# Kernel tuning notes

Hardware: AMD Instinct MI355X
Metric: run time of the kernel (lower is better)

The kernel has to match this reference:

```python
import jax, jax.numpy as jnp
import numpy as np


def _split_feature(x, ns):
    # channel-last split: [b,h,w,c] -> [b*ns*ns, h/ns, w/ns, c]
    b, h, w, c = x.shape
    hn, wn = h // ns, w // ns
    return x.reshape(b, ns, hn, ns, wn, c).transpose(0, 1, 3, 2, 4, 5).reshape(b * ns * ns, hn, wn, c)


def _merge_splits(x, ns):
    # inverse of _split_feature: [b*ns*ns, h, w, c] -> [b, ns*h, ns*w, c]
    b, h, w, c = x.shape
    nb = b // (ns * ns)
    return x.reshape(nb, ns, ns, h, w, c).transpose(0, 1, 3, 2, 4, 5).reshape(nb, ns * h, ns * w, c)


def _gen_shift_window_attn_mask(h, w, ns):
    # numpy replica of _unimatch_generate_shift_window_attn_mask
    wsh, wsw = h // ns, w // ns
    ssh, ssw = wsh // 2, wsw // 2
    img = np.zeros((1, h, w, 1), dtype=np.float32)
    cnt = 0
    for hs in (slice(0, -wsh), slice(-wsh, -ssh), slice(-ssh, None)):
        for ws in (slice(0, -wsw), slice(-wsw, -ssw), slice(-ssw, None)):
            img[:, hs, ws, :] = cnt
            cnt += 1
    win = img.reshape(1, ns, wsh, ns, wsw, 1).transpose(0, 1, 3, 2, 4, 5).reshape(ns * ns, wsh * wsw)
    am = win[:, None, :] - win[:, :, None]
    return np.where(am != 0, np.float32(-100.0), np.float32(0.0)).astype(np.float32)


def setup_inputs() -> dict:
    key = jax.random.key(0)
    B, H, W, C, NS = 8, 96, 128, 128, 4
    kq, kk, kv = jax.random.split(key, 3)
    q = jax.random.normal(kq, (B, H * W, C), jnp.float32)
    k = jax.random.normal(kk, (B, H * W, C), jnp.float32)
    v = jax.random.normal(kv, (B, H * W, C), jnp.float32)
    attn_mask = jnp.asarray(_gen_shift_window_attn_mask(H, W, NS))  # [NS*NS, n, n]
    return {"q": q, "k": k, "v": v, "attn_mask": attn_mask,
            "num_splits": NS, "with_shift": 1, "h": H, "w": W}


def reference(q, k, v, attn_mask, num_splits, with_shift, h, w):
    b, _, c = q.shape
    ns = num_splits
    wsh, wsw = h // ns, w // ns
    n = wsh * wsw
    bn = b * ns * ns
    q = q.reshape(b, h, w, c)
    k = k.reshape(b, h, w, c)
    v = v.reshape(b, h, w, c)
    if with_shift:
        sh, sw = wsh // 2, wsw // 2
        q = jnp.roll(q, (-sh, -sw), axis=(1, 2))
        k = jnp.roll(k, (-sh, -sw), axis=(1, 2))
        v = jnp.roll(v, (-sh, -sw), axis=(1, 2))
    qf = _split_feature(q, ns).reshape(bn, n, c)
    kf = _split_feature(k, ns).reshape(bn, n, c)
    vf = _split_feature(v, ns).reshape(bn, n, c)
    scale = jnp.asarray(c, qf.dtype) ** 0.5
    scores = jnp.einsum('bnc,bmc->bnm', qf, kf) / scale  # [bn, n, n]
    if with_shift:
        scores = scores + jnp.tile(attn_mask, (b, 1, 1))
    attn = jax.nn.softmax(scores, axis=-1)
    out = jnp.einsum('bnm,bmc->bnc', attn, vf)
    out = _merge_splits(out.reshape(bn, wsh, wsw, c), ns)  # [b, h, w, c]
    if with_shift:
        out = jnp.roll(out, (sh, sw), axis=(1, 2))
    return out.reshape(b, h * w, c)
```

## Files before the change

### kernel.cpp

```cpp
#include <hip/hip_runtime.h>

#define H 96
#define W 128
#define C 128
#define WSH 24
#define WSW 32
#define NTOK 768
#define SH 12
#define SW 16
#define KT 32
#define NKT 24
#define PSTR 40
#define TILE_USH 8192
#define WS_NEED (128L * NKT * TILE_USH * 2)

typedef __attribute__((ext_vector_type(8))) short short8;
typedef __attribute__((ext_vector_type(4))) float floatx4;

__device__ inline unsigned short f2bf(float f) {
  union { float f; unsigned u; } un; un.f = f;
  unsigned r = un.u + 0x7FFF + ((un.u >> 16) & 1);
  return (unsigned short)(r >> 16);
}

__device__ inline int tok_off(int tok, int wh, int ww) {
  int r = tok >> 5;
  int cc = tok & 31;
  int y = wh * WSH + r + SH; if (y >= H) y -= H;
  int x = ww * WSW + cc + SW; if (x >= W) x -= W;
  return y * W + x;
}

__global__ __launch_bounds__(256) void prep_kernel(const float* __restrict__ k,
                                                   const float* __restrict__ v,
                                                   unsigned short* __restrict__ ws) {
  __shared__ unsigned short Vlds[KT][136];
  const int bid = blockIdx.x;
  const int w = bid / NKT;
  const int kt = bid - w * NKT;
  const int batch = w >> 4, win = w & 15;
  const int wh = win >> 2, ww = win & 3;
  int y = wh * WSH + kt + SH; if (y >= H) y -= H;

  const int t = threadIdx.x;
  const int key = t >> 3;
  const int j = t & 7;
  const int c0 = j * 16;
  int x = ww * WSW + key + SW; if (x >= W) x -= W;
  const long src = ((long)batch * H * W + (long)y * W + x) * C + c0;
  unsigned short* tile = ws + (long)bid * TILE_USH;

  {
    const float* kp = k + src;
    short8 s0, s1;
#pragma unroll
    for (int i = 0; i < 2; ++i) {
      floatx4 a = *(const floatx4*)(kp + i * 8);
      floatx4 b = *(const floatx4*)(kp + i * 8 + 4);
      s0[i*4+0] = (short)f2bf(a[0]); s0[i*4+1] = (short)f2bf(a[1]);
      s0[i*4+2] = (short)f2bf(a[2]); s0[i*4+3] = (short)f2bf(a[3]);
      s1[i*4+0] = (short)f2bf(b[0]); s1[i*4+1] = (short)f2bf(b[1]);
      s1[i*4+2] = (short)f2bf(b[2]); s1[i*4+3] = (short)f2bf(b[3]);
    }
    short8 o0, o1;
    o0[0]=s0[0]; o0[1]=s0[1]; o0[2]=s0[2]; o0[3]=s0[3]; o0[4]=s1[0]; o0[5]=s1[1]; o0[6]=s1[2]; o0[7]=s1[3];
    o1[0]=s0[4]; o1[1]=s0[5]; o1[2]=s0[6]; o1[3]=s0[7]; o1[4]=s1[4]; o1[5]=s1[5]; o1[6]=s1[6]; o1[7]=s1[7];
    const int kc = j >> 1;
    const int q2 = (j & 1) * 2;
    unsigned short* kout = tile + kc * 1024 + key * 32 + q2 * 8;
    *(short8*)(kout) = o0;
    *(short8*)(kout + 8) = o1;
  }
  {
    const float* vp = v + src;
#pragma unroll
    for (int i = 0; i < 4; ++i) {
      floatx4 a = *(const floatx4*)(vp + i * 4);
      Vlds[key][c0 + i*4 + 0] = f2bf(a[0]);
      Vlds[key][c0 + i*4 + 1] = f2bf(a[1]);
      Vlds[key][c0 + i*4 + 2] = f2bf(a[2]);
      Vlds[key][c0 + i*4 + 3] = f2bf(a[3]);
    }
  }
  __syncthreads();
  {
    const int cb = t >> 5;
    const int rem = t & 31;
    const int col = rem >> 1, qh = rem & 1;
    const int ch = cb * 16 + col;
#pragma unroll
    for (int qs = 0; qs < 2; ++qs) {
      const int quad = qh * 2 + qs;
      short8 o;
#pragma unroll
      for (int i = 0; i < 8; ++i)
        o[i] = (short)Vlds[(i & 1) * 16 + quad * 4 + (i >> 1)][ch];
      *(short8*)(tile + 4096 + cb * 512 + (col * 4 + quad) * 8) = o;
    }
  }
}

__global__ __launch_bounds__(128, 2) void attn_main(const float* __restrict__ q,
                                                    const unsigned short* __restrict__ ws,
                                                    float* __restrict__ out) {
  __shared__ unsigned short Ps[2][3][16 * PSTR];

  const int bid = blockIdx.x;
  const int x8 = bid & 7;
  const int i = bid >> 3;
  const int w = x8 * 16 + (i & 15);
  const int qb = i >> 4;
  const int batch = w >> 4, win = w & 15;
  const int wh = win >> 2, ww = win & 3;

  const int tid = threadIdx.x;
  const int wave = tid >> 6, lane = tid & 63;
  const int col = lane & 15, quad = lane >> 4;
  const long bbase = (long)batch * (H * W * C);
  const int qbase = qb * 96 + wave * 48;
  const int loff = (col * 4 + quad) * 8;

  short8 qfrag[3][4];
#pragma unroll
  for (int s = 0; s < 3; ++s) {
    const int qtok = qbase + s * 16 + col;
    const float* qp = q + bbase + (long)tok_off(qtok, wh, ww) * C + quad * 8;
#pragma unroll
    for (int kc = 0; kc < 4; ++kc) {
      floatx4 a = *(const floatx4*)(qp + kc * 32);
      floatx4 b = *(const floatx4*)(qp + kc * 32 + 4);
      short8 v8;
      v8[0]=(short)f2bf(a[0]); v8[1]=(short)f2bf(a[1]); v8[2]=(short)f2bf(a[2]); v8[3]=(short)f2bf(a[3]);
      v8[4]=(short)f2bf(b[0]); v8[5]=(short)f2bf(b[1]); v8[6]=(short)f2bf(b[2]); v8[7]=(short)f2bf(b[3]);
      qfrag[s][kc] = v8;
    }
  }

  int qreg[3];
#pragma unroll
  for (int s = 0; s < 3; ++s) {
    int t0 = qbase + s * 16;
    int rr_s = t0 >> 5;
    int qh = (wh == 3) ? ((rr_s >= SH) ? 2 : 1) : 0;
    int qw = (ww == 3) ? ((t0 & 16) ? 2 : 1) : 0;
    qreg[s] = qh * 3 + qw;
  }
  const int cw0 = (ww == 3) ? 1 : 0, cw1 = (ww == 3) ? 2 : 0;
  const float MNEG = -144.2695041f;
  const float SC2 = 0.12751739f;

  floatx4 oacc[3][8];
#pragma unroll
  for (int s = 0; s < 3; ++s)
#pragma unroll
    for (int cb = 0; cb < 8; ++cb) oacc[s][cb] = (floatx4){0.f, 0.f, 0.f, 0.f};
  float lsum[3][4];
#pragma unroll
  for (int s = 0; s < 3; ++s)
#pragma unroll
    for (int r = 0; r < 4; ++r) lsum[s][r] = 0.f;

  const unsigned short* wsw_ = ws + (long)w * (NKT * TILE_USH);

  short8 kf0[4], kf1[4];
  auto load_k = [&](int kt) {
    const unsigned short* tk = wsw_ + ((long)kt << 13);
#pragma unroll
    for (int kc = 0; kc < 4; ++kc) {
      kf0[kc] = *(const short8*)(tk + kc * 1024 + loff);
      kf1[kc] = *(const short8*)(tk + kc * 1024 + 512 + loff);
    }
  };
  load_k(0);

  for (int kt = 0; kt < NKT; ++kt) {
    const unsigned short* tv = wsw_ + ((long)kt << 13) + 4096;
    short8 vf[8];
#pragma unroll
    for (int cb = 0; cb < 8; ++cb) vf[cb] = *(const short8*)(tv + cb * 512 + loff);

    const int khb = (wh == 3) ? ((kt >= SH) ? 6 : 3) : 0;
    const int kr0 = khb + cw0, kr1 = khb + cw1;

#pragma unroll
    for (int s = 0; s < 3; ++s) {
      floatx4 a0 = (floatx4){0.f, 0.f, 0.f, 0.f};
      floatx4 a1 = (floatx4){0.f, 0.f, 0.f, 0.f};
#pragma unroll
      for (int kc = 0; kc < 4; ++kc) {
        a0 = __builtin_amdgcn_mfma_f32_16x16x32_bf16(qfrag[s][kc], kf0[kc], a0, 0, 0, 0);
        a1 = __builtin_amdgcn_mfma_f32_16x16x32_bf16(qfrag[s][kc], kf1[kc], a1, 0, 0, 0);
      }
      const float m0 = (qreg[s] == kr0) ? 0.f : MNEG;
      const float m1 = (qreg[s] == kr1) ? 0.f : MNEG;
#pragma unroll
      for (int r = 0; r < 4; ++r) {
        float p0 = __builtin_amdgcn_exp2f(fmaf(a0[r], SC2, m0));
        float p1 = __builtin_amdgcn_exp2f(fmaf(a1[r], SC2, m1));
        lsum[s][r] += p0 + p1;
        unsigned pk = (unsigned)f2bf(p0) | ((unsigned)f2bf(p1) << 16);
        *(unsigned*)&Ps[wave][s][(quad * 4 + r) * PSTR + 2 * col] = pk;
      }
    }

    if (kt + 1 < NKT) load_k(kt + 1);

#pragma unroll
    for (int s = 0; s < 3; ++s) {
      short8 pf = *(const short8*)&Ps[wave][s][col * PSTR + quad * 8];
#pragma unroll
      for (int cb = 0; cb < 8; ++cb)
        oacc[s][cb] = __builtin_amdgcn_mfma_f32_16x16x32_bf16(pf, vf[cb], oacc[s][cb], 0, 0, 0);
    }
  }

#pragma unroll
  for (int s = 0; s < 3; ++s)
#pragma unroll
    for (int r = 0; r < 4; ++r) {
      float l = lsum[s][r];
      l += __shfl_xor(l, 1); l += __shfl_xor(l, 2);
      l += __shfl_xor(l, 4); l += __shfl_xor(l, 8);
      float inv = 1.0f / l;
      int tok = qbase + s * 16 + quad * 4 + r;
      float* op = out + bbase + (long)tok_off(tok, wh, ww) * C + col;
#pragma unroll
      for (int cb = 0; cb < 8; ++cb) op[cb * 16] = oacc[s][cb][r] * inv;
    }
}

#define KSTRF 136
#define VSTRF 40
#define PSTRF 40
__global__ __launch_bounds__(256, 2) void attn_fallback(
    const float* __restrict__ q, const float* __restrict__ k,
    const float* __restrict__ v, const float* __restrict__ mask,
    float* __restrict__ out) {
  __shared__ unsigned short Ks[KT * KSTRF];
  __shared__ unsigned short Vtl[C * VSTRF];
  __shared__ unsigned short Psf[4][16 * PSTRF];
  const int qtile = blockIdx.x;
  const int beta  = blockIdx.y;
  const int batch = beta >> 4;
  const int win   = beta & 15;
  const int wh = win >> 2, ww = win & 3;
  const int tid = threadIdx.x;
  const int wave = tid >> 6, lane = tid & 63;
  const int col = lane & 15, quad = lane >> 4;
  const long bbase = (long)batch * (H * W * C);
  const int qtok = qtile * 64 + wave * 16 + col;
  const float* qp = q + bbase + (long)tok_off(qtok, wh, ww) * C + quad * 8;
  short8 qfrag[4];
#pragma unroll
  for (int kc = 0; kc < 4; ++kc) {
    floatx4 a = *(const floatx4*)(qp + kc * 32);
    floatx4 b = *(const floatx4*)(qp + kc * 32 + 4);
    short8 s;
    s[0]=f2bf(a[0]); s[1]=f2bf(a[1]); s[2]=f2bf(a[2]); s[3]=f2bf(a[3]);
    s[4]=f2bf(b[0]); s[5]=f2bf(b[1]); s[6]=f2bf(b[2]); s[7]=f2bf(b[3]);
    qfrag[kc] = s;
  }
  floatx4 oacc[8];
#pragma unroll
  for (int i = 0; i < 8; ++i) oacc[i] = (floatx4){0.f,0.f,0.f,0.f};
  float mrow[4], lrow[4];
#pragma unroll
  for (int r = 0; r < 4; ++r) { mrow[r] = -1e30f; lrow[r] = 0.f; }
  const int skey = tid >> 3;
  const int sch  = (tid & 7) * 4;
  const float invscale = 0.088388347648318447f;
  const float* maskw = mask + (long)win * (NTOK * NTOK);
  const int qrow_m = qtile * 64 + wave * 16 + quad * 4;
  for (int kt = 0; kt < NKT; ++kt) {
    const int ktok0 = kt * KT;
    const long srow = bbase + (long)tok_off(ktok0 + skey, wh, ww) * C;
    const float* kp = k + srow;
    const float* vp = v + srow;
    __syncthreads();
#pragma unroll
    for (int j = 0; j < 4; ++j) {
      floatx4 f = *(const floatx4*)(kp + sch + j * 32);
      unsigned lo = (unsigned)f2bf(f[0]) | ((unsigned)f2bf(f[1]) << 16);
      unsigned hi = (unsigned)f2bf(f[2]) | ((unsigned)f2bf(f[3]) << 16);
      *(uint2*)&Ks[skey * KSTRF + sch + j * 32] = make_uint2(lo, hi);
    }
#pragma unroll
    for (int j = 0; j < 4; ++j) {
      floatx4 f = *(const floatx4*)(vp + sch + j * 32);
      int chb = sch + j * 32;
      Vtl[(chb + 0) * VSTRF + skey] = f2bf(f[0]);
      Vtl[(chb + 1) * VSTRF + skey] = f2bf(f[1]);
      Vtl[(chb + 2) * VSTRF + skey] = f2bf(f[2]);
      Vtl[(chb + 3) * VSTRF + skey] = f2bf(f[3]);
    }
    __syncthreads();
    floatx4 s0 = (floatx4){0.f,0.f,0.f,0.f};
    floatx4 s1 = (floatx4){0.f,0.f,0.f,0.f};
#pragma unroll
    for (int kc = 0; kc < 4; ++kc) {
      short8 k0 = *(const short8*)&Ks[col * KSTRF + kc * 32 + quad * 8];
      short8 k1 = *(const short8*)&Ks[(col + 16) * KSTRF + kc * 32 + quad * 8];
      s0 = __builtin_amdgcn_mfma_f32_16x16x32_bf16(qfrag[kc], k0, s0, 0, 0, 0);
      s1 = __builtin_amdgcn_mfma_f32_16x16x32_bf16(qfrag[kc], k1, s1, 0, 0, 0);
    }
    float mk0[4], mk1[4];
    const float* mp = maskw + (long)qrow_m * NTOK + ktok0 + col;
#pragma unroll
    for (int r = 0; r < 4; ++r) { mk0[r] = mp[r * NTOK]; mk1[r] = mp[r * NTOK + 16]; }
#pragma unroll
    for (int r = 0; r < 4; ++r) {
      float a0 = s0[r] * invscale + mk0[r];
      float a1 = s1[r] * invscale + mk1[r];
      float mx = fmaxf(a0, a1);
      mx = fmaxf(mx, __shfl_xor(mx, 1)); mx = fmaxf(mx, __shfl_xor(mx, 2));
      mx = fmaxf(mx, __shfl_xor(mx, 4)); mx = fmaxf(mx, __shfl_xor(mx, 8));
      float mnew = fmaxf(mrow[r], mx);
      float alpha = __expf(mrow[r] - mnew);
      float p0 = __expf(a0 - mnew);
      float p1 = __expf(a1 - mnew);
      float rs = p0 + p1;
      rs += __shfl_xor(rs, 1); rs += __shfl_xor(rs, 2);
      rs += __shfl_xor(rs, 4); rs += __shfl_xor(rs, 8);
      lrow[r] = lrow[r] * alpha + rs;
      mrow[r] = mnew;
#pragma unroll
      for (int cb = 0; cb < 8; ++cb) oacc[cb][r] *= alpha;
      Psf[wave][(quad * 4 + r) * PSTRF + col]      = f2bf(p0);
      Psf[wave][(quad * 4 + r) * PSTRF + 16 + col] = f2bf(p1);
    }
    __syncthreads();
    short8 pf = *(const short8*)&Psf[wave][col * PSTRF + quad * 8];
#pragma unroll
    for (int cb = 0; cb < 8; ++cb) {
      short8 vf = *(const short8*)&Vtl[(cb * 16 + col) * VSTRF + quad * 8];
      oacc[cb] = __builtin_amdgcn_mfma_f32_16x16x32_bf16(pf, vf, oacc[cb], 0, 0, 0);
    }
  }
#pragma unroll
  for (int r = 0; r < 4; ++r) {
    float inv_l = 1.0f / lrow[r];
    int tok = qtile * 64 + wave * 16 + quad * 4 + r;
    float* op = out + bbase + (long)tok_off(tok, wh, ww) * C + col;
#pragma unroll
    for (int cb = 0; cb < 8; ++cb) op[cb * 16] = oacc[cb][r] * inv_l;
  }
}

extern "C" void kernel_launch(void* const* d_in, const int* in_sizes, int n_in,
                              void* d_out, int out_size, void* d_ws, size_t ws_size,
                              hipStream_t stream) {
  const float* q    = (const float*)d_in[0];
  const float* k    = (const float*)d_in[1];
  const float* v    = (const float*)d_in[2];
  const float* mask = (const float*)d_in[3];
  float* out = (float*)d_out;
  if (ws_size >= (size_t)WS_NEED) {
    prep_kernel<<<128 * NKT, 256, 0, stream>>>(k, v, (unsigned short*)d_ws);
    attn_main<<<1024, 128, 0, stream>>>(q, (const unsigned short*)d_ws, out);
  } else {
    attn_fallback<<<dim3(12, 128), dim3(256), 0, stream>>>(q, k, v, mask, out);
  }
}
```

Before: 252.9 us.

## Stage K/V tiles into LDS via async global_load_lds with double buffering

The attention kernel now uses 4-wave blocks covering 192 queries. Each key tile (K and V bf16, 16KB) is loaded once per block into double-buffered LDS with global_load_lds, replacing per-wave global loads, and a barrier is placed at the end of each iteration. The prep kernel's block-to-window mapping is remapped so that each XCD handles the same windows, which should improve L2 locality. In exchange the kernel uses more LDS per block, halves the grid to 512 blocks, and waits on vmcnt(0) plus a barrier every iteration, which may serialize the prefetch.

```diff
diff --git a/kernel.cpp b/kernel.cpp
--- a/kernel.cpp
+++ b/kernel.cpp
@@ -31,13 +31,21 @@
   return y * W + x;
 }
 
+__device__ inline void gll16(const void* g, void* lds) {
+  __builtin_amdgcn_global_load_lds(
+      (const __attribute__((address_space(1))) unsigned int*)g,
+      (__attribute__((address_space(3))) unsigned int*)lds, 16, 0, 0);
+}
+
 __global__ __launch_bounds__(256) void prep_kernel(const float* __restrict__ k,
                                                    const float* __restrict__ v,
                                                    unsigned short* __restrict__ ws) {
   __shared__ unsigned short Vlds[KT][136];
   const int bid = blockIdx.x;
-  const int w = bid / NKT;
-  const int kt = bid - w * NKT;
+  const int xcd = bid & 7;
+  const int jj = bid >> 3;
+  const int w = xcd * 16 + (jj & 15);
+  const int kt = jj >> 4;
   const int batch = w >> 4, win = w & 15;
   const int wh = win >> 2, ww = win & 3;
   int y = wh * WSH + kt + SH; if (y >= H) y -= H;
@@ -48,7 +56,7 @@
   const int c0 = j * 16;
   int x = ww * WSW + key + SW; if (x >= W) x -= W;
   const long src = ((long)batch * H * W + (long)y * W + x) * C + c0;
-  unsigned short* tile = ws + (long)bid * TILE_USH;
+  unsigned short* tile = ws + ((long)w * NKT + kt) * TILE_USH;
 
   {
     const float* kp = k + src;
@@ -100,10 +108,11 @@
   }
 }
 
-__global__ __launch_bounds__(128, 2) void attn_main(const float* __restrict__ q,
+__global__ __launch_bounds__(256, 2) void attn_main(const float* __restrict__ q,
                                                     const unsigned short* __restrict__ ws,
                                                     float* __restrict__ out) {
-  __shared__ unsigned short Ps[2][3][16 * PSTR];
+  __shared__ unsigned short Kv[2][TILE_USH];
+  __shared__ unsigned short Ps[4][3][16 * PSTR];
 
   const int bid = blockIdx.x;
   const int x8 = bid & 7;
@@ -114,11 +123,24 @@
   const int wh = win >> 2, ww = win & 3;
 
   const int tid = threadIdx.x;
-  const int wave = tid >> 6, lane = tid & 63;
+  const int wv = tid >> 6, lane = tid & 63;
   const int col = lane & 15, quad = lane >> 4;
   const long bbase = (long)batch * (H * W * C);
-  const int qbase = qb * 96 + wave * 48;
+  const int qbase = qb * 192 + wv * 48;
   const int loff = (col * 4 + quad) * 8;
+
+  const char* wtile = (const char*)(ws + (long)w * (NKT * TILE_USH));
+
+  auto stage = [&](int buf, int kt) {
+    const char* g = wtile + ((long)kt << 14);
+#pragma unroll
+    for (int c = 0; c < 4; ++c) {
+      const int chunk = wv * 4 + c;
+      gll16(g + chunk * 1024 + lane * 16, &Kv[buf][chunk * 512]);
+    }
+  };
+
+  stage(0, 0);
 
   short8 qfrag[3][4];
 #pragma unroll
@@ -160,24 +182,19 @@
 #pragma unroll
     for (int r = 0; r < 4; ++r) lsum[s][r] = 0.f;
 
-  const unsigned short* wsw_ = ws + (long)w * (NKT * TILE_USH);
-
-  short8 kf0[4], kf1[4];
-  auto load_k = [&](int kt) {
-    const unsigned short* tk = wsw_ + ((long)kt << 13);
+  asm volatile("s_waitcnt vmcnt(0)" ::: "memory");
+  __builtin_amdgcn_s_barrier();
+
+  for (int kt = 0; kt < NKT; ++kt) {
+    const int cur = kt & 1;
+    if (kt + 1 < NKT) stage(cur ^ 1, kt + 1);
+
+    short8 kf0[4], kf1[4];
 #pragma unroll
     for (int kc = 0; kc < 4; ++kc) {
-      kf0[kc] = *(const short8*)(tk + kc * 1024 + loff);
-      kf1[kc] = *(const short8*)(tk + kc * 1024 + 512 + loff);
-    }
-  };
-  load_k(0);
-
-  for (int kt = 0; kt < NKT; ++kt) {
-    const unsigned short* tv = wsw_ + ((long)kt << 13) + 4096;
-    short8 vf[8];
-#pragma unroll
-    for (int cb = 0; cb < 8; ++cb) vf[cb] = *(const short8*)(tv + cb * 512 + loff);
+      kf0[kc] = *(const short8*)&Kv[cur][kc * 1024 + loff];
+      kf1[kc] = *(const short8*)&Kv[cur][kc * 1024 + 512 + loff];
+    }
 
     const int khb = (wh == 3) ? ((kt >= SH) ? 6 : 3) : 0;
     const int kr0 = khb + cw0, kr1 = khb + cw1;
@@ -199,18 +216,26 @@
         float p1 = __builtin_amdgcn_exp2f(fmaf(a1[r], SC2, m1));
         lsum[s][r] += p0 + p1;
         unsigned pk = (unsigned)f2bf(p0) | ((unsigned)f2bf(p1) << 16);
-        *(unsigned*)&Ps[wave][s][(quad * 4 + r) * PSTR + 2 * col] = pk;
+        *(unsigned*)&Ps[wv][s][(quad * 4 + r) * PSTR + 2 * col] = pk;
       }
     }
 
-    if (kt + 1 < NKT) load_k(kt + 1);
+    short8 vf[8];
+#pragma unroll
+    for (int cb = 0; cb < 8; ++cb)
+      vf[cb] = *(const short8*)&Kv[cur][4096 + cb * 512 + loff];
 
 #pragma unroll
     for (int s = 0; s < 3; ++s) {
-      short8 pf = *(const short8*)&Ps[wave][s][col * PSTR + quad * 8];
+      short8 pf = *(const short8*)&Ps[wv][s][col * PSTR + quad * 8];
 #pragma unroll
       for (int cb = 0; cb < 8; ++cb)
         oacc[s][cb] = __builtin_amdgcn_mfma_f32_16x16x32_bf16(pf, vf[cb], oacc[s][cb], 0, 0, 0);
+    }
+
+    if (kt + 1 < NKT) {
+      asm volatile("s_waitcnt vmcnt(0)" ::: "memory");
+      __builtin_amdgcn_s_barrier();
     }
   }
 
@@ -356,7 +381,7 @@
   float* out = (float*)d_out;
   if (ws_size >= (size_t)WS_NEED) {
     prep_kernel<<<128 * NKT, 256, 0, stream>>>(k, v, (unsigned short*)d_ws);
-    attn_main<<<1024, 128, 0, stream>>>(q, (const unsigned short*)d_ws, out);
+    attn_main<<<512, 256, 0, stream>>>(q, (const unsigned short*)d_ws, out);
   } else {
     attn_fallback<<<dim3(12, 128), dim3(256), 0, stream>>>(q, k, v, mask, out);
   }
```

New measurement: 254.3 us. No clear change (+0.5%).
